# Kernel optimization log

Measured on AMD Instinct MI355X. Metric: run time of the kernel, lower is better.

The kernel has to match this reference:

```python
import jax, jax.numpy as jnp
import numpy as np

B, N, DIM = 2, 2048, 1024
HEADS, DH = 16, 64
INNER = HEADS * DH
LN_EPS = 1e-5


def setup_inputs() -> dict:
    key = jax.random.key(0)
    ks = jax.random.split(key, 3)
    x = jax.random.normal(ks[0], (B, N, DIM), dtype=jnp.float32)
    ln_w = jnp.ones((DIM,), dtype=jnp.float32)
    ln_b = jnp.zeros((DIM,), dtype=jnp.float32)
    w_qkv = jax.random.normal(ks[1], (DIM, 3 * INNER), dtype=jnp.float32) * (DIM ** -0.5)
    w_out = jax.random.normal(ks[2], (INNER, DIM), dtype=jnp.float32) * (INNER ** -0.5)
    b_out = jnp.zeros((DIM,), dtype=jnp.float32)
    return {"x": x, "ln_w": ln_w, "ln_b": ln_b, "w_qkv": w_qkv, "w_out": w_out, "b_out": b_out}


def _rope(q, k):
    # q, k: (b, h, n, d) with d even; interleaved RoPE matching the torch module.
    n, d = q.shape[-2], q.shape[-1]
    inv_freq = jnp.exp(jnp.arange(0, d, 2, dtype=jnp.float32) * (-jnp.log(jnp.float32(10000.0)) / d))
    ang = jnp.arange(n, dtype=jnp.float32)[:, None] * inv_freq[None, :]  # (n, d/2)
    cos = jnp.repeat(jnp.cos(ang), 2, axis=-1)  # (n, d) -> broadcast over b,h
    sin = jnp.repeat(jnp.sin(ang), 2, axis=-1)

    def rot(t):
        t2 = t.reshape(*t.shape[:-1], d // 2, 2)  # pairs (even, odd)
        t2 = jnp.stack([-t2[..., 1], t2[..., 0]], axis=-1).reshape(t.shape)
        return t * cos + t2 * sin

    return rot(q), rot(k)


def reference(x, ln_w, ln_b, w_qkv, w_out, b_out):
    # LayerNorm
    mu = jnp.mean(x, axis=-1, keepdims=True)
    var = jnp.var(x, axis=-1, keepdims=True)
    xn = (x - mu) * jax.lax.rsqrt(var + LN_EPS) * ln_w + ln_b
    # QKV projection (no bias)
    qkv = xn @ w_qkv  # (b, n, 3*inner)
    q, k, v = jnp.split(qkv, 3, axis=-1)
    split_heads = lambda t: t.reshape(B, N, HEADS, DH).transpose(0, 2, 1, 3)  # b h n d
    q, k, v = split_heads(q), split_heads(k), split_heads(v)
    q, k = _rope(q, k)
    scale = DH ** -0.5
    dots = jnp.einsum('bhid,bhjd->bhij', q, k) * scale
    attn = jax.nn.softmax(dots, axis=-1)
    out = jnp.einsum('bhij,bhjd->bhid', attn, v)
    out = out.transpose(0, 2, 1, 3).reshape(B, N, INNER)  # b n (h d)
    return out @ w_out + b_out
```

## Files before the change

kernel.cpp:

```cpp
#include <hip/hip_runtime.h>

typedef unsigned short u16;
typedef unsigned int   u32;
typedef __bf16 bf16x8 __attribute__((ext_vector_type(8)));
typedef __bf16 bf16x2 __attribute__((ext_vector_type(2)));
typedef float  f32x4  __attribute__((ext_vector_type(4)));

#define B_     2
#define N_     2048
#define DIM_   1024
#define HEADS_ 16
#define DH_    64
#define BH_    (B_*HEADS_)
#define ROWS_  (B_*N_)

__device__ __forceinline__ u16 f2b(float f) {
  union { __bf16 h; u16 u; } v; v.h = (__bf16)f; return v.u;
}
__device__ __forceinline__ u32 pkb(float a, float b) {
  bf16x2 t; t[0] = (__bf16)a; t[1] = (__bf16)b;
  union { bf16x2 v; u32 u; } c; c.v = t; return c.u;
}
__device__ __forceinline__ float b2f(u16 h) {
  union { u32 u; float f; } v; v.u = ((u32)h) << 16;
  return v.f;
}
__device__ __forceinline__ void gload16(const void* g, void* l) {
  __builtin_amdgcn_global_load_lds(
      (const __attribute__((address_space(1))) void*)g,
      (__attribute__((address_space(3))) void*)l, 16, 0, 0);
}
__device__ __forceinline__ f32x4 mfma16(bf16x8 a, bf16x8 b, f32x4 c) {
  return __builtin_amdgcn_mfma_f32_16x16x32_bf16(a, b, c, 0, 0, 0);
}

__global__ __launch_bounds__(256) void ln_kernel(const float* __restrict__ x,
    const float* __restrict__ lw, const float* __restrict__ lb,
    u16* __restrict__ xn) {
  int r = blockIdx.x, t = threadIdx.x;
  const float4* xr = (const float4*)(x + (size_t)r * DIM_);
  float4 v = xr[t];
  float s  = v.x + v.y + v.z + v.w;
  float s2 = v.x*v.x + v.y*v.y + v.z*v.z + v.w*v.w;
  #pragma unroll
  for (int off = 32; off >= 1; off >>= 1) {
    s  += __shfl_down(s, off);
    s2 += __shfl_down(s2, off);
  }
  __shared__ float ps[4], ps2[4], bc[2];
  int w = t >> 6, lane = t & 63;
  if (lane == 0) { ps[w] = s; ps2[w] = s2; }
  __syncthreads();
  if (t == 0) {
    float S = ps[0]+ps[1]+ps[2]+ps[3], S2 = ps2[0]+ps2[1]+ps2[2]+ps2[3];
    float mu = S * (1.0f/DIM_);
    float var = S2 * (1.0f/DIM_) - mu*mu;
    bc[0] = mu; bc[1] = rsqrtf(var + 1e-5f);
  }
  __syncthreads();
  float mu = bc[0], rs = bc[1];
  float4 wv = ((const float4*)lw)[t];
  float4 bv = ((const float4*)lb)[t];
  u32 lo = pkb((v.x-mu)*rs*wv.x + bv.x, (v.y-mu)*rs*wv.y + bv.y);
  u32 hi = pkb((v.z-mu)*rs*wv.z + bv.z, (v.w-mu)*rs*wv.w + bv.w);
  ((uint2*)xn)[(size_t)r*256 + t] = make_uint2(lo, hi);
}

__global__ __launch_bounds__(256) void transpose_f32_bf16(const float* __restrict__ in,
    u16* __restrict__ out, int R, int C) {
  __shared__ float tile[32][33];
  int tx = threadIdx.x & 31, ty = threadIdx.x >> 5;
  int c0 = blockIdx.x * 32, r0 = blockIdx.y * 32;
  #pragma unroll
  for (int i = 0; i < 4; i++)
    tile[ty + i*8][tx] = in[(size_t)(r0 + ty + i*8) * C + c0 + tx];
  __syncthreads();
  #pragma unroll
  for (int i = 0; i < 4; i++)
    out[(size_t)(c0 + ty + i*8) * R + r0 + tx] = f2b(tile[tx][ty + i*8]);
}

template<int MODE>
__global__ __launch_bounds__(256) void gemm_bt(
    const u16* __restrict__ A, const u16* __restrict__ Bt, int N, int K,
    u16* __restrict__ qo, u16* __restrict__ ko, u16* __restrict__ vo,
    const float* __restrict__ bias, float* __restrict__ out) {
  __shared__ __align__(16) u16 lA[128*32];
  __shared__ __align__(16) u16 lB[128*32];
  int tid = threadIdx.x;
  int lane = tid & 63;
  int w = tid >> 6, wm = w >> 1, wn = w & 1;
  int l15 = lane & 15, g = lane >> 4;
  int bm = blockIdx.x, bn = blockIdx.y;
  const f32x4 z = {0.f, 0.f, 0.f, 0.f};
  f32x4 acc[4][4];
  #pragma unroll
  for (int i = 0; i < 4; i++)
    #pragma unroll
    for (int j = 0; j < 4; j++)
      acc[i][j] = z;
  const u16* ag = A  + (size_t)(bm*128 + (tid>>2)) * K + (tid&3)*8;
  const u16* bg = Bt + (size_t)(bn*128 + (tid>>2)) * K + (tid&3)*8;
  u16* la = lA + tid*8;
  u16* lb = lB + tid*8;
  for (int k0 = 0; k0 < K; k0 += 32) {
    gload16(ag + k0,                la);
    gload16(ag + (size_t)64*K + k0, la + 2048);
    gload16(bg + k0,                lb);
    gload16(bg + (size_t)64*K + k0, lb + 2048);
    __syncthreads();
    bf16x8 af[4], bfr[4];
    #pragma unroll
    for (int mt = 0; mt < 4; mt++)
      af[mt] = *(const bf16x8*)(lA + (wm*64 + mt*16 + l15)*32 + g*8);
    #pragma unroll
    for (int nt = 0; nt < 4; nt++)
      bfr[nt] = *(const bf16x8*)(lB + (wn*64 + nt*16 + l15)*32 + g*8);
    __builtin_amdgcn_s_setprio(1);
    #pragma unroll
    for (int mt = 0; mt < 4; mt++)
      #pragma unroll
      for (int nt = 0; nt < 4; nt++)
        acc[mt][nt] = mfma16(af[mt], bfr[nt], acc[mt][nt]);
    __builtin_amdgcn_s_setprio(0);
    __syncthreads();
  }
  #pragma unroll
  for (int mt = 0; mt < 4; mt++) {
    #pragma unroll
    for (int nt = 0; nt < 4; nt++) {
      #pragma unroll
      for (int reg = 0; reg < 4; reg++) {
        int rr = bm*128 + wm*64 + mt*16 + g*4 + reg;
        int cc = bn*128 + wn*64 + nt*16 + l15;
        float val = acc[mt][nt][reg];
        if (MODE == 0) {
          int which = cc >> 10, inner = cc & 1023;
          int h = inner >> 6, dd = inner & 63;
          int b = rr >> 11, np = rr & 2047;
          int bh = b*HEADS_ + h;
          if (which == 0)      qo[((size_t)(bh*2048 + np))*64 + dd] = f2b(val);
          else if (which == 1) ko[((size_t)(bh*2048 + np))*64 + dd] = f2b(val);
          else                 vo[((size_t)(bh*64 + dd))*2048 + np] = f2b(val);
        } else {
          out[(size_t)rr * N + cc] = val + bias[cc];
        }
      }
    }
  }
}

__global__ __launch_bounds__(256) void rope_kernel(u16* q, u16* k) {
  int tid = blockIdx.x * 256 + threadIdx.x;
  int row = tid >> 3, sub = tid & 7;
  int n = row & 2047;
  u32* qp = (u32*)(q + (size_t)row * 64 + sub * 8);
  u32* kp = (u32*)(k + (size_t)row * 64 + sub * 8);
  uint4 uq = *(uint4*)qp;
  uint4 uk = *(uint4*)kp;
  float c4[4], s4[4];
  #pragma unroll
  for (int j = 0; j < 4; j++) {
    int p = sub*4 + j;
    float freq = expf(-(2.0f * (float)p) * (9.210340371976184f / 64.0f));
    float ang = (float)n * freq;
    __sincosf(ang, &s4[j], &c4[j]);
  }
  const float qs = 0.125f * 1.4426950408889634f;
#define ROPE_Q(u, c, s) { \
    float e = b2f((u16)(u)), o = b2f((u16)((u) >> 16)); \
    (u) = pkb((e*(c) - o*(s))*qs, (o*(c) + e*(s))*qs); }
#define ROPE_K(u, c, s) { \
    float e = b2f((u16)(u)), o = b2f((u16)((u) >> 16)); \
    (u) = pkb(e*(c) - o*(s), o*(c) + e*(s)); }
  ROPE_Q(uq.x, c4[0], s4[0]) ROPE_Q(uq.y, c4[1], s4[1])
  ROPE_Q(uq.z, c4[2], s4[2]) ROPE_Q(uq.w, c4[3], s4[3])
  ROPE_K(uk.x, c4[0], s4[0]) ROPE_K(uk.y, c4[1], s4[1])
  ROPE_K(uk.z, c4[2], s4[2]) ROPE_K(uk.w, c4[3], s4[3])
#undef ROPE_Q
#undef ROPE_K
  *(uint4*)qp = uq;
  *(uint4*)kp = uk;
}

__global__ __launch_bounds__(512) void flash_attn(
    const u16* __restrict__ qbf, const u16* __restrict__ kbf,
    const u16* __restrict__ vt, u16* __restrict__ aout) {
  __shared__ __align__(16) char lK[3][8192];
  __shared__ __align__(16) char lV[3][8192];
  __shared__ __align__(16) char pl[8][2048];
  int tid = threadIdx.x;
  int w = tid >> 6, lane = tid & 63;
  int l15 = lane & 15, g = lane >> 4;
  int lin = blockIdx.x;
  int nb = (lin & 7) * 64 + (lin >> 3);
  int bh = nb >> 4, qb = nb & 15;
  const f32x4 z = {0.f, 0.f, 0.f, 0.f};
  const u16* qbase = qbf + ((size_t)bh*2048 + qb*128 + w*16) * 64;
  bf16x8 qa0 = *(const bf16x8*)(qbase + l15*64 + g*8);
  bf16x8 qa1 = *(const bf16x8*)(qbase + l15*64 + 32 + g*8);
  const char* kb = (const char*)(kbf + (size_t)bh * 2048 * 64);
  const char* vb = (const char*)(vt  + (size_t)bh * 64 * 2048);
  int srow = tid >> 3;
  int sb   = (tid & 7) * 16;
  int soff = sb ^ ((srow & 7) << 4);
  char* pw = pl[w];
  const int swz = (l15 & 7) << 4;

  float lp[4] = {0.f, 0.f, 0.f, 0.f};
  f32x4 o[4];
  #pragma unroll
  for (int i = 0; i < 4; i++) o[i] = z;

#define STAGE(t, buf) { \
    gload16(kb + (size_t)((t)*64 + srow) * 128 + soff, &lK[buf][(size_t)tid*16]); \
    gload16(vb + (size_t)srow * 4096 + (t)*128 + soff, &lV[buf][(size_t)tid*16]); }

  STAGE(0, 0)
  STAGE(1, 1)
  asm volatile("s_waitcnt vmcnt(2)" ::: "memory");
  __builtin_amdgcn_s_barrier();

  int cur = 0, pfb = 2;
  #pragma unroll 1
  for (int t = 0; t < 32; ++t) {
    if (t < 30) STAGE(t + 2, pfb)
    const char* Kc = lK[cur];
    const char* Vc = lV[cur];
    f32x4 st[4];
    __builtin_amdgcn_s_setprio(1);
    #pragma unroll
    for (int kt = 0; kt < 4; kt++) {
      const char* krow = Kc + (kt*16 + l15) * 128;
      bf16x8 k0 = *(const bf16x8*)(krow + ((g*16) ^ swz));
      bf16x8 k1 = *(const bf16x8*)(krow + ((64 + g*16) ^ swz));
      f32x4 a = mfma16(k0, qa0, z);
      st[kt] = mfma16(k1, qa1, a);
    }
    __builtin_amdgcn_s_setprio(0);
    #pragma unroll
    for (int kt = 0; kt < 4; kt++)
      #pragma unroll
      for (int r = 0; r < 4; r++) {
        float p = __builtin_amdgcn_exp2f(st[kt][r]);
        st[kt][r] = p;
        lp[kt] += p;
      }
    #pragma unroll
    for (int kt = 0; kt < 4; kt++) {
      u32 lo = pkb(st[kt][0], st[kt][1]);
      u32 hi = pkb(st[kt][2], st[kt][3]);
      *(uint2*)(pw + l15*128 + ((kt*32 + g*8) ^ swz)) = make_uint2(lo, hi);
    }
    bf16x8 pb0 = *(const bf16x8*)(pw + l15*128 + ((g*16) ^ swz));
    bf16x8 pb1 = *(const bf16x8*)(pw + l15*128 + ((64 + g*16) ^ swz));
    __builtin_amdgcn_s_setprio(1);
    #pragma unroll
    for (int dt = 0; dt < 4; dt++) {
      const char* vrow = Vc + (dt*16 + l15) * 128;
      bf16x8 v0 = *(const bf16x8*)(vrow + ((g*16) ^ swz));
      bf16x8 v1 = *(const bf16x8*)(vrow + ((64 + g*16) ^ swz));
      o[dt] = mfma16(v0, pb0, o[dt]);
      o[dt] = mfma16(v1, pb1, o[dt]);
    }
    __builtin_amdgcn_s_setprio(0);
    if (t < 31) {
      if (t < 30) { asm volatile("s_waitcnt vmcnt(2)" ::: "memory"); }
      else        { asm volatile("s_waitcnt vmcnt(0)" ::: "memory"); }
      __builtin_amdgcn_s_barrier();
    }
    cur = (cur + 1 == 3) ? 0 : cur + 1;
    pfb = (pfb + 1 == 3) ? 0 : pfb + 1;
  }
#undef STAGE

  float lsp = (lp[0] + lp[1]) + (lp[2] + lp[3]);
  lsp += __shfl_xor(lsp, 16);
  lsp += __shfl_xor(lsp, 32);
  float rls = 1.0f / lsp;

  #pragma unroll
  for (int dt = 0; dt < 4; dt++)
    #pragma unroll
    for (int r = 0; r < 4; r++) {
      int d = dt*16 + g*4 + r;
      *(u16*)(pw + l15*128 + ((d*2) ^ swz)) = f2b(o[dt][r] * rls);
    }
  int b = bh >> 4, h = bh & 15;
  int rl = lane >> 3;
  #pragma unroll
  for (int i = 0; i < 2; i++) {
    int row = i*8 + rl;
    uint4 ov = *(const uint4*)(pw + row*128 + (((lane & 7)*16) ^ (rl << 4)));
    int n = qb*128 + w*16 + row;
    *(uint4*)(aout + ((size_t)(b*2048 + n))*1024 + h*64 + (lane & 7)*8) = ov;
  }
}

extern "C" void kernel_launch(void* const* d_in, const int* in_sizes, int n_in,
                              void* d_out, int out_size, void* d_ws, size_t ws_size,
                              hipStream_t stream) {
  const float* x    = (const float*)d_in[0];
  const float* lw   = (const float*)d_in[1];
  const float* lb   = (const float*)d_in[2];
  const float* wqkv = (const float*)d_in[3];
  const float* wout = (const float*)d_in[4];
  const float* bout = (const float*)d_in[5];
  float* out = (float*)d_out;

  char* ws = (char*)d_ws;
  size_t off = 0;
  auto alloc = [&](size_t bytes) {
    char* p = ws + off;
    off += (bytes + 255) & ~(size_t)255;
    return p;
  };
  u16* xn   = (u16*)alloc((size_t)ROWS_*DIM_*2);
  u16* wqt  = (u16*)alloc((size_t)3072*1024*2);
  u16* wot  = (u16*)alloc((size_t)1024*1024*2);
  u16* qb   = (u16*)alloc((size_t)BH_*2048*64*2);
  u16* kb   = (u16*)alloc((size_t)BH_*2048*64*2);
  u16* vtb  = (u16*)alloc((size_t)BH_*2048*64*2);
  u16* aout = (u16*)alloc((size_t)ROWS_*1024*2);

  ln_kernel<<<ROWS_, 256, 0, stream>>>(x, lw, lb, xn);
  transpose_f32_bf16<<<dim3(96, 32), 256, 0, stream>>>(wqkv, wqt, 1024, 3072);
  transpose_f32_bf16<<<dim3(32, 32), 256, 0, stream>>>(wout, wot, 1024, 1024);
  gemm_bt<0><<<dim3(32, 24), 256, 0, stream>>>(xn, wqt, 3072, 1024,
                                               qb, kb, vtb, nullptr, nullptr);
  rope_kernel<<<2048, 256, 0, stream>>>(qb, kb);
  flash_attn<<<512, 512, 0, stream>>>(qb, kb, vtb, aout);
  gemm_bt<1><<<dim3(32, 8), 256, 0, stream>>>(aout, wot, 1024, 1024,
                                              nullptr, nullptr, nullptr, bout, out);
}
```

Baseline: 132.2 us.

## Permute K rows to keep P in registers and widen GEMM K-step

In the attention kernel, K rows are loaded into LDS in a permuted order so that the MFMA output layout of the score tile lines up directly with the B-operand layout of the PV MFMA. This lets the exp'd probabilities be packed into bf16x8 in registers, removing the LDS write/read round trip for P. The projection GEMM now loads two 32-wide K slices per barrier pair, halving the number of syncs per K, at the cost of twice the LDS per block, which may reduce occupancy.

```diff
diff --git a/kernel.cpp b/kernel.cpp
--- a/kernel.cpp
+++ b/kernel.cpp
@@ -85,8 +85,8 @@
     const u16* __restrict__ A, const u16* __restrict__ Bt, int N, int K,
     u16* __restrict__ qo, u16* __restrict__ ko, u16* __restrict__ vo,
     const float* __restrict__ bias, float* __restrict__ out) {
-  __shared__ __align__(16) u16 lA[128*32];
-  __shared__ __align__(16) u16 lB[128*32];
+  __shared__ __align__(16) u16 lA[2][128*32];
+  __shared__ __align__(16) u16 lB[2][128*32];
   int tid = threadIdx.x;
   int lane = tid & 63;
   int w = tid >> 6, wm = w >> 1, wn = w & 1;
@@ -101,28 +101,34 @@
       acc[i][j] = z;
   const u16* ag = A  + (size_t)(bm*128 + (tid>>2)) * K + (tid&3)*8;
   const u16* bg = Bt + (size_t)(bn*128 + (tid>>2)) * K + (tid&3)*8;
-  u16* la = lA + tid*8;
-  u16* lb = lB + tid*8;
-  for (int k0 = 0; k0 < K; k0 += 32) {
-    gload16(ag + k0,                la);
-    gload16(ag + (size_t)64*K + k0, la + 2048);
-    gload16(bg + k0,                lb);
-    gload16(bg + (size_t)64*K + k0, lb + 2048);
+  int lo8 = tid*8;
+  for (int k0 = 0; k0 < K; k0 += 64) {
+    gload16(ag + k0,                     &lA[0][lo8]);
+    gload16(ag + (size_t)64*K + k0,      &lA[0][lo8 + 2048]);
+    gload16(bg + k0,                     &lB[0][lo8]);
+    gload16(bg + (size_t)64*K + k0,      &lB[0][lo8 + 2048]);
+    gload16(ag + k0 + 32,                &lA[1][lo8]);
+    gload16(ag + (size_t)64*K + k0 + 32, &lA[1][lo8 + 2048]);
+    gload16(bg + k0 + 32,                &lB[1][lo8]);
+    gload16(bg + (size_t)64*K + k0 + 32, &lB[1][lo8 + 2048]);
     __syncthreads();
-    bf16x8 af[4], bfr[4];
-    #pragma unroll
-    for (int mt = 0; mt < 4; mt++)
-      af[mt] = *(const bf16x8*)(lA + (wm*64 + mt*16 + l15)*32 + g*8);
-    #pragma unroll
-    for (int nt = 0; nt < 4; nt++)
-      bfr[nt] = *(const bf16x8*)(lB + (wn*64 + nt*16 + l15)*32 + g*8);
-    __builtin_amdgcn_s_setprio(1);
-    #pragma unroll
-    for (int mt = 0; mt < 4; mt++)
+    #pragma unroll
+    for (int half = 0; half < 2; half++) {
+      bf16x8 af[4], bfr[4];
+      #pragma unroll
+      for (int mt = 0; mt < 4; mt++)
+        af[mt] = *(const bf16x8*)(&lA[half][(wm*64 + mt*16 + l15)*32 + g*8]);
       #pragma unroll
       for (int nt = 0; nt < 4; nt++)
-        acc[mt][nt] = mfma16(af[mt], bfr[nt], acc[mt][nt]);
-    __builtin_amdgcn_s_setprio(0);
+        bfr[nt] = *(const bf16x8*)(&lB[half][(wn*64 + nt*16 + l15)*32 + g*8]);
+      __builtin_amdgcn_s_setprio(1);
+      #pragma unroll
+      for (int mt = 0; mt < 4; mt++)
+        #pragma unroll
+        for (int nt = 0; nt < 4; nt++)
+          acc[mt][nt] = mfma16(af[mt], bfr[nt], acc[mt][nt]);
+      __builtin_amdgcn_s_setprio(0);
+    }
     __syncthreads();
   }
   #pragma unroll
@@ -202,8 +208,9 @@
   const char* kb = (const char*)(kbf + (size_t)bh * 2048 * 64);
   const char* vb = (const char*)(vt  + (size_t)bh * 64 * 2048);
   int srow = tid >> 3;
-  int sb   = (tid & 7) * 16;
-  int soff = sb ^ ((srow & 7) << 4);
+  int soff = ((tid & 7) * 16) ^ ((srow & 7) << 4);
+  int ksrc = (srow & 32) | (((srow >> 2) & 3) << 3)
+           | (((srow >> 4) & 1) << 2) | (srow & 3);
   char* pw = pl[w];
   const int swz = (l15 & 7) << 4;
 
@@ -213,7 +220,7 @@
   for (int i = 0; i < 4; i++) o[i] = z;
 
 #define STAGE(t, buf) { \
-    gload16(kb + (size_t)((t)*64 + srow) * 128 + soff, &lK[buf][(size_t)tid*16]); \
+    gload16(kb + (size_t)((t)*64 + ksrc) * 128 + soff, &lK[buf][(size_t)tid*16]); \
     gload16(vb + (size_t)srow * 4096 + (t)*128 + soff, &lV[buf][(size_t)tid*16]); }
 
   STAGE(0, 0)
@@ -246,22 +253,20 @@
         st[kt][r] = p;
         lp[kt] += p;
       }
-    #pragma unroll
-    for (int kt = 0; kt < 4; kt++) {
-      u32 lo = pkb(st[kt][0], st[kt][1]);
-      u32 hi = pkb(st[kt][2], st[kt][3]);
-      *(uint2*)(pw + l15*128 + ((kt*32 + g*8) ^ swz)) = make_uint2(lo, hi);
-    }
-    bf16x8 pb0 = *(const bf16x8*)(pw + l15*128 + ((g*16) ^ swz));
-    bf16x8 pb1 = *(const bf16x8*)(pw + l15*128 + ((64 + g*16) ^ swz));
     __builtin_amdgcn_s_setprio(1);
     #pragma unroll
-    for (int dt = 0; dt < 4; dt++) {
-      const char* vrow = Vc + (dt*16 + l15) * 128;
-      bf16x8 v0 = *(const bf16x8*)(vrow + ((g*16) ^ swz));
-      bf16x8 v1 = *(const bf16x8*)(vrow + ((64 + g*16) ^ swz));
-      o[dt] = mfma16(v0, pb0, o[dt]);
-      o[dt] = mfma16(v1, pb1, o[dt]);
+    for (int h = 0; h < 2; h++) {
+      union { u32 u[4]; bf16x8 v; } pf;
+      pf.u[0] = pkb(st[2*h][0],   st[2*h][1]);
+      pf.u[1] = pkb(st[2*h][2],   st[2*h][3]);
+      pf.u[2] = pkb(st[2*h+1][0], st[2*h+1][1]);
+      pf.u[3] = pkb(st[2*h+1][2], st[2*h+1][3]);
+      #pragma unroll
+      for (int dt = 0; dt < 4; dt++) {
+        const char* vrow = Vc + (dt*16 + l15) * 128;
+        bf16x8 vf = *(const bf16x8*)(vrow + ((h*64 + g*16) ^ swz));
+        o[dt] = mfma16(vf, pf.v, o[dt]);
+      }
     }
     __builtin_amdgcn_s_setprio(0);
     if (t < 31) {
```

Measured after the change: 128.3 us. -2.9%, faster.

## Split KV tile across wave pairs with register-resident P and LDS reduction

Applied to the files above, without the earlier changes.

Reorganizes flash attention so each wave handles 32 query rows and half of each 64-key tile, with waves split by key half (rho) and query group (p). K rows are permuted during staging so the S MFMA output layout feeds directly as the B operand of the PV MFMA, removing the per-iteration LDS round trip for P. Partial outputs and row sums from the two key halves are combined through shared memory at the end. This raises register reuse of K/V fragments, adds an epilogue reduction with several barriers, and requests higher occupancy via launch bounds.

```diff
diff --git a/kernel.cpp b/kernel.cpp
--- a/kernel.cpp
+++ b/kernel.cpp
@@ -183,38 +183,46 @@
   *(uint4*)kp = uk;
 }
 
-__global__ __launch_bounds__(512) void flash_attn(
+__global__ __launch_bounds__(512, 4) void flash_attn(
     const u16* __restrict__ qbf, const u16* __restrict__ kbf,
     const u16* __restrict__ vt, u16* __restrict__ aout) {
-  __shared__ __align__(16) char lK[3][8192];
-  __shared__ __align__(16) char lV[3][8192];
-  __shared__ __align__(16) char pl[8][2048];
+  __shared__ __align__(16) char smem[49152];
+  char* lK = smem;
+  char* lV = smem + 24576;
   int tid = threadIdx.x;
   int w = tid >> 6, lane = tid & 63;
   int l15 = lane & 15, g = lane >> 4;
+  int p = w & 3, rho = w >> 2;
   int lin = blockIdx.x;
   int nb = (lin & 7) * 64 + (lin >> 3);
   int bh = nb >> 4, qb = nb & 15;
   const f32x4 z = {0.f, 0.f, 0.f, 0.f};
-  const u16* qbase = qbf + ((size_t)bh*2048 + qb*128 + w*16) * 64;
-  bf16x8 qa0 = *(const bf16x8*)(qbase + l15*64 + g*8);
-  bf16x8 qa1 = *(const bf16x8*)(qbase + l15*64 + 32 + g*8);
+  const u16* qrow_base = qbf + ((size_t)bh*2048 + qb*128 + p*32) * 64;
+  bf16x8 Qf[2][2];
+  #pragma unroll
+  for (int qt = 0; qt < 2; qt++)
+    #pragma unroll
+    for (int dh = 0; dh < 2; dh++)
+      Qf[qt][dh] = *(const bf16x8*)(qrow_base + (qt*16 + l15)*64 + dh*32 + g*8);
   const char* kb = (const char*)(kbf + (size_t)bh * 2048 * 64);
   const char* vb = (const char*)(vt  + (size_t)bh * 64 * 2048);
   int srow = tid >> 3;
-  int sb   = (tid & 7) * 16;
-  int soff = sb ^ ((srow & 7) << 4);
-  char* pw = pl[w];
+  int soff = ((tid & 7) * 16) ^ ((srow & 7) << 4);
+  int sl = srow & 31;
+  int ksrc = (srow & 32) | (((sl >> 2) & 3) << 3) | (((sl >> 4) & 1) << 2) | (sl & 3);
   const int swz = (l15 & 7) << 4;
 
-  float lp[4] = {0.f, 0.f, 0.f, 0.f};
-  f32x4 o[4];
-  #pragma unroll
-  for (int i = 0; i < 4; i++) o[i] = z;
+  float lp[2][2] = {{0.f, 0.f}, {0.f, 0.f}};
+  f32x4 o[4][2];
+  #pragma unroll
+  for (int i = 0; i < 4; i++)
+    #pragma unroll
+    for (int j = 0; j < 2; j++)
+      o[i][j] = z;
 
 #define STAGE(t, buf) { \
-    gload16(kb + (size_t)((t)*64 + srow) * 128 + soff, &lK[buf][(size_t)tid*16]); \
-    gload16(vb + (size_t)srow * 4096 + (t)*128 + soff, &lV[buf][(size_t)tid*16]); }
+    gload16(kb + (size_t)((t)*64 + ksrc) * 128 + soff, lK + (buf)*8192 + (size_t)tid*16); \
+    gload16(vb + (size_t)srow * 4096 + (t)*128 + soff, lV + (buf)*8192 + (size_t)tid*16); }
 
   STAGE(0, 0)
   STAGE(1, 1)
@@ -225,43 +233,50 @@
   #pragma unroll 1
   for (int t = 0; t < 32; ++t) {
     if (t < 30) STAGE(t + 2, pfb)
-    const char* Kc = lK[cur];
-    const char* Vc = lV[cur];
-    f32x4 st[4];
+    const char* Kc = lK + cur*8192;
+    const char* Vc = lV + cur*8192;
+    f32x4 st[2][2];
+    bf16x8 ka[2][2];
+    #pragma unroll
+    for (int kt = 0; kt < 2; kt++)
+      #pragma unroll
+      for (int dh = 0; dh < 2; dh++)
+        ka[kt][dh] = *(const bf16x8*)(Kc + (rho*32 + kt*16 + l15)*128
+                                         + ((dh*64 + g*16) ^ swz));
     __builtin_amdgcn_s_setprio(1);
     #pragma unroll
-    for (int kt = 0; kt < 4; kt++) {
-      const char* krow = Kc + (kt*16 + l15) * 128;
-      bf16x8 k0 = *(const bf16x8*)(krow + ((g*16) ^ swz));
-      bf16x8 k1 = *(const bf16x8*)(krow + ((64 + g*16) ^ swz));
-      f32x4 a = mfma16(k0, qa0, z);
-      st[kt] = mfma16(k1, qa1, a);
-    }
+    for (int kt = 0; kt < 2; kt++)
+      #pragma unroll
+      for (int qt = 0; qt < 2; qt++) {
+        f32x4 a = mfma16(ka[kt][0], Qf[qt][0], z);
+        st[kt][qt] = mfma16(ka[kt][1], Qf[qt][1], a);
+      }
     __builtin_amdgcn_s_setprio(0);
     #pragma unroll
-    for (int kt = 0; kt < 4; kt++)
-      #pragma unroll
-      for (int r = 0; r < 4; r++) {
-        float p = __builtin_amdgcn_exp2f(st[kt][r]);
-        st[kt][r] = p;
-        lp[kt] += p;
-      }
-    #pragma unroll
-    for (int kt = 0; kt < 4; kt++) {
-      u32 lo = pkb(st[kt][0], st[kt][1]);
-      u32 hi = pkb(st[kt][2], st[kt][3]);
-      *(uint2*)(pw + l15*128 + ((kt*32 + g*8) ^ swz)) = make_uint2(lo, hi);
-    }
-    bf16x8 pb0 = *(const bf16x8*)(pw + l15*128 + ((g*16) ^ swz));
-    bf16x8 pb1 = *(const bf16x8*)(pw + l15*128 + ((64 + g*16) ^ swz));
+    for (int kt = 0; kt < 2; kt++)
+      #pragma unroll
+      for (int qt = 0; qt < 2; qt++)
+        #pragma unroll
+        for (int r = 0; r < 4; r++) {
+          float pv = __builtin_amdgcn_exp2f(st[kt][qt][r]);
+          st[kt][qt][r] = pv;
+          lp[qt][kt] += pv;
+        }
+    bf16x8 vf[4];
+    #pragma unroll
+    for (int dt = 0; dt < 4; dt++)
+      vf[dt] = *(const bf16x8*)(Vc + (dt*16 + l15)*128 + ((rho*64 + g*16) ^ swz));
     __builtin_amdgcn_s_setprio(1);
     #pragma unroll
-    for (int dt = 0; dt < 4; dt++) {
-      const char* vrow = Vc + (dt*16 + l15) * 128;
-      bf16x8 v0 = *(const bf16x8*)(vrow + ((g*16) ^ swz));
-      bf16x8 v1 = *(const bf16x8*)(vrow + ((64 + g*16) ^ swz));
-      o[dt] = mfma16(v0, pb0, o[dt]);
-      o[dt] = mfma16(v1, pb1, o[dt]);
+    for (int qt = 0; qt < 2; qt++) {
+      union { u32 u[4]; bf16x8 v; } pf;
+      pf.u[0] = pkb(st[0][qt][0], st[0][qt][1]);
+      pf.u[1] = pkb(st[0][qt][2], st[0][qt][3]);
+      pf.u[2] = pkb(st[1][qt][0], st[1][qt][1]);
+      pf.u[3] = pkb(st[1][qt][2], st[1][qt][3]);
+      #pragma unroll
+      for (int dt = 0; dt < 4; dt++)
+        o[dt][qt] = mfma16(vf[dt], pf.v, o[dt][qt]);
     }
     __builtin_amdgcn_s_setprio(0);
     if (t < 31) {
@@ -274,26 +289,69 @@
   }
 #undef STAGE
 
-  float lsp = (lp[0] + lp[1]) + (lp[2] + lp[3]);
-  lsp += __shfl_xor(lsp, 16);
-  lsp += __shfl_xor(lsp, 32);
-  float rls = 1.0f / lsp;
-
-  #pragma unroll
-  for (int dt = 0; dt < 4; dt++)
-    #pragma unroll
-    for (int r = 0; r < 4; r++) {
-      int d = dt*16 + g*4 + r;
-      *(u16*)(pw + l15*128 + ((d*2) ^ swz)) = f2b(o[dt][r] * rls);
+  float ls[2];
+  #pragma unroll
+  for (int qt = 0; qt < 2; qt++) {
+    ls[qt] = lp[qt][0] + lp[qt][1];
+    ls[qt] += __shfl_xor(ls[qt], 16);
+    ls[qt] += __shfl_xor(ls[qt], 32);
+  }
+  __syncthreads();
+
+  float* lspx = (float*)(smem + 32768);
+  if (rho == 1) {
+    #pragma unroll
+    for (int dt = 0; dt < 4; dt++)
+      #pragma unroll
+      for (int qt = 0; qt < 2; qt++) {
+        int ql = qt*16 + l15;
+        int off = p*8192 + ql*256 + ((dt*64 + g*16) ^ ((ql & 7) << 4));
+        *(f32x4*)(smem + off) = o[dt][qt];
+      }
+    if (g == 0) {
+      lspx[p*64 + l15]      = ls[0];
+      lspx[p*64 + 16 + l15] = ls[1];
     }
+  }
+  __syncthreads();
+  float rls[2] = {0.f, 0.f};
+  if (rho == 0) {
+    #pragma unroll
+    for (int qt = 0; qt < 2; qt++)
+      rls[qt] = 1.0f / (ls[qt] + lspx[p*64 + qt*16 + l15]);
+    #pragma unroll
+    for (int dt = 0; dt < 4; dt++)
+      #pragma unroll
+      for (int qt = 0; qt < 2; qt++) {
+        int ql = qt*16 + l15;
+        int off = p*8192 + ql*256 + ((dt*64 + g*16) ^ ((ql & 7) << 4));
+        o[dt][qt] += *(const f32x4*)(smem + off);
+      }
+  }
+  __syncthreads();
+  if (rho == 0) {
+    #pragma unroll
+    for (int dt = 0; dt < 4; dt++)
+      #pragma unroll
+      for (int qt = 0; qt < 2; qt++) {
+        int ql = qt*16 + l15;
+        u32 w0 = pkb(o[dt][qt][0]*rls[qt], o[dt][qt][1]*rls[qt]);
+        u32 w1 = pkb(o[dt][qt][2]*rls[qt], o[dt][qt][3]*rls[qt]);
+        int d2 = dt*32 + g*8;
+        *(uint2*)(smem + p*8192 + ql*128 + (d2 ^ ((ql & 7) << 4))) =
+            make_uint2(w0, w1);
+      }
+  }
+  __syncthreads();
+  int row = tid >> 2;
   int b = bh >> 4, h = bh & 15;
-  int rl = lane >> 3;
-  #pragma unroll
-  for (int i = 0; i < 2; i++) {
-    int row = i*8 + rl;
-    uint4 ov = *(const uint4*)(pw + row*128 + (((lane & 7)*16) ^ (rl << 4)));
-    int n = qb*128 + w*16 + row;
-    *(uint4*)(aout + ((size_t)(b*2048 + n))*1024 + h*64 + (lane & 7)*8) = ov;
+  int n = qb*128 + row;
+  #pragma unroll
+  for (int j = 0; j < 2; j++) {
+    int slot = (tid & 3)*2 + j;
+    uint4 rv = *(const uint4*)(smem + (row >> 5)*8192 + (row & 31)*128
+                               + ((slot*16) ^ ((row & 7) << 4)));
+    *(uint4*)(aout + ((size_t)(b*2048 + n))*1024 + h*64 + slot*8) = rv;
   }
 }
 
```

Measured after the change: 124.5 us. -5.8%, faster.
